# Performance work log

Hardware: AMD Instinct MI355X
Metric: run time of the kernel (lower is better)

The kernel has to match this reference:

```python
import jax, jax.numpy as jnp
import numpy as np

ALPHA = 0.7
EPS = 1e-12


def setup_inputs() -> dict:
    key = jax.random.key(0)
    k1, k2, k3, k4 = jax.random.split(key, 4)
    B, P, D = 4, 256, 384  # dinov2_vits14: 224/14=16 -> 256 patches, dim 384
    N, M = 100000, 2000    # local memory bank (max_memory), global bank (train images)
    return {
        "patches": jax.random.normal(k1, (B, P, D), dtype=jnp.float32),
        "globals_x": jax.random.normal(k2, (B, D), dtype=jnp.float32),
        "mb_local": jax.random.normal(k3, (N, D), dtype=jnp.float32),
        "mb_global": jax.random.normal(k4, (M, D), dtype=jnp.float32),
    }


def _l2_normalize(x):
    return x / (jnp.linalg.norm(x, axis=-1, keepdims=True) + EPS)


def reference(patches, globals_x, mb_local, mb_global):
    # Token normalization as in _extract_patch_tokens / _extract_global
    p = _l2_normalize(patches)    # [B, P, D]
    g = _l2_normalize(globals_x)  # [B, D]

    # Local: Euclidean cdist(p_i, MB_local) via gram trick, min over bank, max over patches
    p_sq = jnp.sum(p * p, axis=-1)                      # [B, P]
    mbl_sq = jnp.sum(mb_local * mb_local, axis=-1)      # [N]
    d2 = (p_sq[..., None] + mbl_sq[None, None, :]
          - 2.0 * jnp.einsum('bpd,nd->bpn', p, mb_local))  # [B, P, N]
    d = jnp.sqrt(jnp.maximum(d2, 0.0))
    local_score = jnp.max(jnp.min(d, axis=2), axis=1)   # [B]

    # Global: cdist(g_i, MB_global).min()
    g_sq = jnp.sum(g * g, axis=-1)                      # [B]
    mbg_sq = jnp.sum(mb_global * mb_global, axis=-1)    # [M]
    gd2 = g_sq[:, None] + mbg_sq[None, :] - 2.0 * (g @ mb_global.T)  # [B, M]
    gdist = jnp.min(jnp.sqrt(jnp.maximum(gd2, 0.0)), axis=1)         # [B]

    return ALPHA * local_score + (1.0 - ALPHA) * gdist  # [B] anomaly scores
```

## Files before the change

kernel.cpp:

```cpp
#include <hip/hip_runtime.h>
#include <math.h>


#define D 384
#define PQ 256
#define TNP 128
#define BK 64
#define LROW 72

typedef __attribute__((ext_vector_type(8))) short short8v;
typedef __attribute__((ext_vector_type(4))) float f32x4;

static __device__ __forceinline__ unsigned short f2bf(float f) {
  unsigned u = __float_as_uint(f);
  unsigned r = 0x7FFFu + ((u >> 16) & 1u);
  return (unsigned short)((u + r) >> 16);
}
static __device__ __forceinline__ unsigned pack2(float lo, float hi) {
  return (unsigned)f2bf(lo) | ((unsigned)f2bf(hi) << 16);
}

__global__ void prep_kernel(const float* __restrict__ patches,
                            const float* __restrict__ globals_x,
                            float* __restrict__ pf32,
                            unsigned short* __restrict__ pbf,
                            float* __restrict__ psq,
                            float* __restrict__ gf32,
                            float* __restrict__ gsq,
                            int Q) {
  const int row = blockIdx.x;
  const int lane = threadIdx.x;
  const float* src = (row < Q) ? (patches + (size_t)row * D)
                               : (globals_x + (size_t)(row - Q) * D);
  float v[6];
  float ss = 0.f;
#pragma unroll
  for (int j = 0; j < 6; ++j) { v[j] = src[lane + 64 * j]; ss += v[j] * v[j]; }
#pragma unroll
  for (int d = 1; d < 64; d <<= 1) ss += __shfl_xor(ss, d);
  const float inv = 1.f / (sqrtf(ss) + 1e-12f);
  float pn[6]; float ps = 0.f;
#pragma unroll
  for (int j = 0; j < 6; ++j) { pn[j] = v[j] * inv; ps += pn[j] * pn[j]; }
#pragma unroll
  for (int d = 1; d < 64; d <<= 1) ps += __shfl_xor(ps, d);
  if (row < Q) {
#pragma unroll
    for (int j = 0; j < 6; ++j) {
      pf32[(size_t)row * D + lane + 64 * j] = pn[j];
      pbf[(size_t)row * D + lane + 64 * j] = f2bf(pn[j]);
    }
    if (lane == 0) psq[row] = ps;
  } else {
    const int b = row - Q;
#pragma unroll
    for (int j = 0; j < 6; ++j) gf32[(size_t)b * D + lane + 64 * j] = pn[j];
    if (lane == 0) gsq[b] = ps;
  }
}

__device__ __forceinline__ void atomic_fmin(float* addr, float val) {
  unsigned* ua = (unsigned*)addr;
  float cur = __uint_as_float(atomicAdd(ua, 0u));
  while (val < cur) {
    unsigned assumed = __float_as_uint(cur);
    unsigned old = atomicCAS(ua, assumed, __float_as_uint(val));
    if (old == assumed) break;
    cur = __uint_as_float(old);
  }
}

template <int MODE>
__global__ __launch_bounds__(256, 2) void score_kernel(
    const float* __restrict__ mbl,
    const unsigned short* __restrict__ pbf,
    float* __restrict__ tilemin,
    int Q, int N, int QP, int q8, int r8) {
  __shared__ alignas(16) unsigned short lB0[TNP * LROW];
  __shared__ alignas(16) unsigned short lB1[TNP * LROW];
  __shared__ float msqH[TNP * 2];
  __shared__ float msqF[TNP];

  const int tid = threadIdx.x;
  const int lane = tid & 63;
  const int wid = tid >> 6;
  const int fr = lane & 15;
  const int g = lane >> 4;

  const int flat = blockIdx.x;
  const int xcd = flat & 7, idx = flat >> 3;
  const int wg = (xcd < r8 ? xcd * (q8 + 1) : r8 * (q8 + 1) + (xcd - r8) * q8) + idx;
  const int nb = wg / QP;
  const int qp = wg - nb * QP;
  const int qbase = qp * PQ;
  const int nbase = nb * TNP;

  const int brow = tid >> 1, h = tid & 1;
  const int gn = nbase + brow;
  const float* bptr = mbl + (size_t)((gn < N) ? gn : 0) * D + h * 32;
  const int boff = brow * LROW + h * 32;

  const unsigned short* abase = pbf + (size_t)(qbase + wid * 64 + fr) * D + g * 8;

  f32x4 acc[4][8];
#pragma unroll
  for (int i = 0; i < 4; ++i)
#pragma unroll
    for (int j = 0; j < 8; ++j) acc[i][j] = (f32x4){0.f, 0.f, 0.f, 0.f};
  float msqreg = 0.f;
  float4 breg[8];
  short8v a[8];

  auto bload = [&](int kc) {
    const float* src = bptr + kc * BK;
#pragma unroll
    for (int i = 0; i < 8; ++i) breg[i] = *(const float4*)(src + i * 4);
  };
  auto bwrite = [&](unsigned short* base) {
    float s = 0.f;
    uint4 w[4];
#pragma unroll
    for (int i = 0; i < 4; ++i) {
      float4 f0 = breg[2 * i], f1 = breg[2 * i + 1];
      s += f0.x*f0.x + f0.y*f0.y + f0.z*f0.z + f0.w*f0.w
         + f1.x*f1.x + f1.y*f1.y + f1.z*f1.z + f1.w*f1.w;
      w[i] = (uint4){ pack2(f0.x,f0.y), pack2(f0.z,f0.w), pack2(f1.x,f1.y), pack2(f1.z,f1.w) };
    }
#pragma unroll
    for (int i = 0; i < 4; ++i) *(uint4*)(base + boff + i * 8) = w[i];
    msqreg += s;
  };
  auto aload = [&](int kc) {
#pragma unroll
    for (int ks = 0; ks < 2; ++ks)
#pragma unroll
      for (int mf = 0; mf < 4; ++mf)
        a[ks * 4 + mf] = *(const short8v*)(abase + (size_t)mf * 16 * D + kc * BK + ks * 32);
  };
  auto compute = [&](const unsigned short* buf) {
#pragma unroll
    for (int ks = 0; ks < 2; ++ks) {
      short8v b[8];
#pragma unroll
      for (int nf = 0; nf < 8; ++nf)
        b[nf] = *(const short8v*)(&buf[(nf * 16 + fr) * LROW + (ks * 4 + g) * 8]);
#pragma unroll
      for (int mf = 0; mf < 4; ++mf)
#pragma unroll
        for (int nf = 0; nf < 8; ++nf)
          acc[mf][nf] = __builtin_amdgcn_mfma_f32_16x16x32_bf16(a[ks * 4 + mf], b[nf],
                                                                acc[mf][nf], 0, 0, 0);
    }
  };

  bload(0);
  bwrite(lB0);
  __syncthreads();
  aload(0); bload(1); compute(lB0); bwrite(lB1); __syncthreads();
  aload(1); bload(2); compute(lB1); bwrite(lB0); __syncthreads();
  aload(2); bload(3); compute(lB0); bwrite(lB1); __syncthreads();
  aload(3); bload(4); compute(lB1); bwrite(lB0); __syncthreads();
  aload(4); bload(5); compute(lB0); bwrite(lB1); __syncthreads();
  aload(5);           compute(lB1);              __syncthreads();

  msqH[tid] = msqreg;
  __syncthreads();
  if (tid < TNP) msqF[tid] = (nbase + tid < N) ? (msqH[2 * tid] + msqH[2 * tid + 1]) : 1e30f;
  __syncthreads();

  float mq[8];
#pragma unroll
  for (int nf = 0; nf < 8; ++nf) mq[nf] = msqF[nf * 16 + fr];

#pragma unroll
  for (int mf = 0; mf < 4; ++mf) {
#pragma unroll
    for (int j = 0; j < 4; ++j) {
      float v[4];
#pragma unroll
      for (int s = 0; s < 4; ++s)
        v[s] = fminf(mq[2 * s] - 2.f * acc[mf][2 * s][j],
                     mq[2 * s + 1] - 2.f * acc[mf][2 * s + 1][j]);
#pragma unroll
      for (int d2 = 1; d2 < 16; d2 <<= 1)
#pragma unroll
        for (int s = 0; s < 4; ++s) v[s] = fminf(v[s], __shfl_xor(v[s], d2));
      if (fr == 0) {
        const int q = qbase + wid * 64 + mf * 16 + g * 4 + j;
        if (MODE == 0) {
#pragma unroll
          for (int s = 0; s < 4; ++s)
            tilemin[(size_t)(nb * 4 + s) * Q + q] = v[s];
        } else {
          atomic_fmin(&tilemin[q],
                      fminf(fminf(v[0], v[1]), fminf(v[2], v[3])));
        }
      }
    }
  }
}

__global__ void init_inf_kernel(float* __restrict__ p, int n) {
  int i = blockIdx.x * 256 + threadIdx.x;
  if (i < n) p[i] = 1e30f;
}
__global__ void final_dmin_kernel(const float* __restrict__ d2min,
                                  const float* __restrict__ psq,
                                  float* __restrict__ dmin, int Q) {
  int q = blockIdx.x * 256 + threadIdx.x;
  if (q < Q) dmin[q] = sqrtf(fmaxf(psq[q] + d2min[q], 0.f));
}

__global__ __launch_bounds__(256) void transpose_kernel(
    const float* __restrict__ tm, float* __restrict__ tmT, int Q, int NSUBP) {
  __shared__ float t[64][65];
  const int tx = threadIdx.x & 63, ty = threadIdx.x >> 6;
  const int qb = blockIdx.x * 64, sb = blockIdx.y * 64;
#pragma unroll
  for (int i = 0; i < 64; i += 4)
    t[i + ty][tx] = tm[(size_t)(sb + i + ty) * Q + qb + tx];
  __syncthreads();
#pragma unroll
  for (int i = 0; i < 64; i += 4)
    tmT[(size_t)(qb + i + ty) * NSUBP + sb + tx] = t[tx][i + ty];
}

__device__ __forceinline__ float block_min(float v, float* red) {
#pragma unroll
  for (int d = 1; d < 64; d <<= 1) v = fminf(v, __shfl_xor(v, d));
  if ((threadIdx.x & 63) == 0) red[threadIdx.x >> 6] = v;
  __syncthreads();
  const float r = fminf(fminf(red[0], red[1]), fminf(red[2], red[3]));
  __syncthreads();
  return r;
}
__device__ __forceinline__ float block_max(float v, float* red) {
#pragma unroll
  for (int d = 1; d < 64; d <<= 1) v = fmaxf(v, __shfl_xor(v, d));
  if ((threadIdx.x & 63) == 0) red[threadIdx.x >> 6] = v;
  __syncthreads();
  const float r = fmaxf(fmaxf(red[0], red[1]), fmaxf(red[2], red[3]));
  __syncthreads();
  return r;
}

__global__ __launch_bounds__(256) void refine_kernel(
    const float* __restrict__ mbl,
    const float* __restrict__ pf32,
    const float* __restrict__ psq,
    const float* __restrict__ tmT,
    float* __restrict__ dmin,
    int Q, int N, int NSUB, int NSUBP) {
  __shared__ int cnt;
  __shared__ int cand[64];
  __shared__ float red[4];
  const int q = blockIdx.x;
  const int tid = threadIdx.x;
  if (tid == 0) cnt = 0;
  __syncthreads();

  const float* rowp = tmT + (size_t)q * NSUBP;
  float m = 1e30f;
  for (int r = tid; r < NSUB; r += 256) m = fminf(m, rowp[r]);
  const float gm = block_min(m, red);
  const float thr = gm + 0.25f;

  for (int r = tid; r < NSUB; r += 256)
    if (rowp[r] <= thr) { int i = atomicAdd(&cnt, 1); if (i < 64) cand[i] = r; }
  __syncthreads();
  const int nc = min(cnt, 64);

  const int row8 = tid >> 3, oct = tid & 7;
  const float* prow = pf32 + (size_t)q * D + oct * 48;
  float4 pr[12];
#pragma unroll
  for (int i = 0; i < 12; ++i) pr[i] = *(const float4*)(prow + i * 4);

  float best = 1e30f;
  for (int c = 0; c < nc; ++c) {
    const int n = cand[c] * 32 + row8;
    float v;
    if (n < N) {
      const float* mr = mbl + (size_t)n * D + oct * 48;
      float dot = 0.f, ms = 0.f;
#pragma unroll
      for (int i = 0; i < 12; ++i) {
        float4 aa = *(const float4*)(mr + i * 4);
        dot += aa.x*pr[i].x + aa.y*pr[i].y + aa.z*pr[i].z + aa.w*pr[i].w;
        ms  += aa.x*aa.x + aa.y*aa.y + aa.z*aa.z + aa.w*aa.w;
      }
      v = ms - 2.f * dot;
    } else {
      v = 1e30f;
    }
#pragma unroll
    for (int d2 = 1; d2 < 8; d2 <<= 1) {
      float o = __shfl_xor(v, d2);
      v = (n < N) ? v + o : 1e30f;
    }
    best = fminf(best, v);
  }
  best = block_min(best, red);
  if (tid == 0) dmin[q] = sqrtf(fmaxf(psq[q] + best, 0.f));
}

__global__ __launch_bounds__(256) void gmin_kernel(
    const float* __restrict__ mbg,
    const float* __restrict__ gf32,
    const float* __restrict__ gsq,
    float* __restrict__ gpartG,
    int M) {
  __shared__ float red[4];
  const int b = blockIdx.x, s = blockIdx.y;
  const int tid = threadIdx.x;
  const int sl = (M + 31) / 32;
  const int row = s * sl + tid;
  const float* g = gf32 + (size_t)b * D;
  float v = 1e30f;
  if (tid < sl && row < M) {
    const float* mr = mbg + (size_t)row * D;
    float dot = 0.f, ms = 0.f;
#pragma unroll 4
    for (int k = 0; k < D; k += 4) {
      float4 aa = *(const float4*)(mr + k);
      float4 p = *(const float4*)(g + k);
      dot += aa.x*p.x + aa.y*p.y + aa.z*p.z + aa.w*p.w;
      ms  += aa.x*aa.x + aa.y*aa.y + aa.z*aa.z + aa.w*aa.w;
    }
    v = gsq[b] + ms - 2.f * dot;
  }
  v = block_min(v, red);
  if (tid == 0) gpartG[b * 32 + s] = v;
}

__global__ __launch_bounds__(256) void out_kernel(
    const float* __restrict__ gpartG,
    const float* __restrict__ dmin,
    float* __restrict__ out,
    int P) {
  __shared__ float red[4];
  const int b = blockIdx.x;
  const int tid = threadIdx.x;
  float v = (tid < P) ? dmin[(size_t)b * P + tid] : -1e30f;
  const float local = block_max(v, red);
  float gm = (tid < 32) ? gpartG[b * 32 + tid] : 1e30f;
  gm = block_min(gm, red);
  if (tid == 0) out[b] = 0.7f * local + 0.3f * sqrtf(fmaxf(gm, 0.f));
}

extern "C" void kernel_launch(void* const* d_in, const int* in_sizes, int n_in,
                              void* d_out, int out_size, void* d_ws, size_t ws_size,
                              hipStream_t stream) {
  const float* patches   = (const float*)d_in[0];
  const float* globals_x = (const float*)d_in[1];
  const float* mbl       = (const float*)d_in[2];
  const float* mbg       = (const float*)d_in[3];
  float* out = (float*)d_out;

  const int Q = in_sizes[0] / D;
  const int B = in_sizes[1] / D;
  const int N = in_sizes[2] / D;
  const int M = in_sizes[3] / D;
  const int P = Q / B;
  const int NPAN = (N + TNP - 1) / TNP;
  const int NSUB = NPAN * 4;
  const int NSUBP = ((NSUB + 63) / 64) * 64;
  const int QP = (Q + PQ - 1) / PQ;
  const int nwg = QP * NPAN;
  const int q8 = nwg / 8, r8 = nwg % 8;

  char* w = (char*)d_ws;
  char* wend = (char*)d_ws + ws_size;
  auto alloc = [&](size_t bytes) {
    char* p = w;
    w += (bytes + 255) & ~(size_t)255;
    return p;
  };
  float*          pf32   = (float*)alloc((size_t)Q * D * sizeof(float));
  unsigned short* pbf    = (unsigned short*)alloc((size_t)Q * D * sizeof(unsigned short));
  float*          psq    = (float*)alloc((size_t)Q * sizeof(float));
  float*          gf32   = (float*)alloc((size_t)B * D * sizeof(float));
  float*          gsqp   = (float*)alloc((size_t)B * sizeof(float));
  float*          dmin   = (float*)alloc((size_t)Q * sizeof(float));
  float*          gpartG = (float*)alloc((size_t)B * 32 * sizeof(float));
  float*          d2min  = (float*)alloc((size_t)Q * sizeof(float));
  if (w > wend) return;

  const size_t tm_bytes = (size_t)NSUBP * Q * sizeof(float);
  const int full = (w + 2 * ((tm_bytes + 255) & ~(size_t)255) <= wend) ? 1 : 0;

  prep_kernel<<<Q + B, 64, 0, stream>>>(patches, globals_x, pf32, pbf, psq, gf32, gsqp, Q);

  if (full) {
    float* tilemin  = (float*)alloc(tm_bytes);
    float* tileminT = (float*)alloc(tm_bytes);
    score_kernel<0><<<nwg, 256, 0, stream>>>(mbl, pbf, tilemin, Q, N, QP, q8, r8);
    transpose_kernel<<<dim3(Q / 64, NSUBP / 64), 256, 0, stream>>>(tilemin, tileminT, Q, NSUBP);
    refine_kernel<<<Q, 256, 0, stream>>>(mbl, pf32, psq, tileminT, dmin, Q, N, NSUB, NSUBP);
  } else {
    init_inf_kernel<<<(Q + 255) / 256, 256, 0, stream>>>(d2min, Q);
    score_kernel<1><<<nwg, 256, 0, stream>>>(mbl, pbf, d2min, Q, N, QP, q8, r8);
    final_dmin_kernel<<<(Q + 255) / 256, 256, 0, stream>>>(d2min, psq, dmin, Q);
  }

  gmin_kernel<<<dim3(B, 32), 256, 0, stream>>>(mbg, gf32, gsqp, gpartG, M);
  out_kernel<<<B, 256, 0, stream>>>(gpartG, dmin, out, P);
}
```

Baseline: 491.7 us.

## Write tile minima in query-major layout and drop the transpose kernel

The score kernel now stores its four per-subtile minima as one float4 per query row, in query-major order, so the refine kernel can read them directly. This removes the separate transpose kernel, its extra buffer, and one full write and read of the tile-min matrix. The B-fragment loads in the MFMA loop are also split into two halves of four to cut live registers. The float4 stores are strided across queries and may coalesce less well than the old row-contiguous writes.

Result: faster. 457.4 us (-7.0%).

```diff
diff --git a/kernel.cpp b/kernel.cpp
--- a/kernel.cpp
+++ b/kernel.cpp
@@ -75,7 +75,7 @@
     const float* __restrict__ mbl,
     const unsigned short* __restrict__ pbf,
     float* __restrict__ tilemin,
-    int Q, int N, int QP, int q8, int r8) {
+    int Q, int N, int NSUBP, int QP, int q8, int r8) {
   __shared__ alignas(16) unsigned short lB0[TNP * LROW];
   __shared__ alignas(16) unsigned short lB1[TNP * LROW];
   __shared__ float msqH[TNP * 2];
@@ -140,16 +140,19 @@
   auto compute = [&](const unsigned short* buf) {
 #pragma unroll
     for (int ks = 0; ks < 2; ++ks) {
-      short8v b[8];
-#pragma unroll
-      for (int nf = 0; nf < 8; ++nf)
-        b[nf] = *(const short8v*)(&buf[(nf * 16 + fr) * LROW + (ks * 4 + g) * 8]);
-#pragma unroll
-      for (int mf = 0; mf < 4; ++mf)
-#pragma unroll
-        for (int nf = 0; nf < 8; ++nf)
-          acc[mf][nf] = __builtin_amdgcn_mfma_f32_16x16x32_bf16(a[ks * 4 + mf], b[nf],
-                                                                acc[mf][nf], 0, 0, 0);
+#pragma unroll
+      for (int half = 0; half < 2; ++half) {
+        short8v b4[4];
+#pragma unroll
+        for (int nf = 0; nf < 4; ++nf)
+          b4[nf] = *(const short8v*)(&buf[((half * 4 + nf) * 16 + fr) * LROW + (ks * 4 + g) * 8]);
+#pragma unroll
+        for (int mf = 0; mf < 4; ++mf)
+#pragma unroll
+          for (int nf = 0; nf < 4; ++nf)
+            acc[mf][half * 4 + nf] = __builtin_amdgcn_mfma_f32_16x16x32_bf16(
+                a[ks * 4 + mf], b4[nf], acc[mf][half * 4 + nf], 0, 0, 0);
+      }
     }
   };
 
@@ -188,9 +191,8 @@
       if (fr == 0) {
         const int q = qbase + wid * 64 + mf * 16 + g * 4 + j;
         if (MODE == 0) {
-#pragma unroll
-          for (int s = 0; s < 4; ++s)
-            tilemin[(size_t)(nb * 4 + s) * Q + q] = v[s];
+          *(float4*)&tilemin[(size_t)q * NSUBP + nb * 4] =
+              (float4){v[0], v[1], v[2], v[3]};
         } else {
           atomic_fmin(&tilemin[q],
                       fminf(fminf(v[0], v[1]), fminf(v[2], v[3])));
@@ -211,20 +213,6 @@
   if (q < Q) dmin[q] = sqrtf(fmaxf(psq[q] + d2min[q], 0.f));
 }
 
-__global__ __launch_bounds__(256) void transpose_kernel(
-    const float* __restrict__ tm, float* __restrict__ tmT, int Q, int NSUBP) {
-  __shared__ float t[64][65];
-  const int tx = threadIdx.x & 63, ty = threadIdx.x >> 6;
-  const int qb = blockIdx.x * 64, sb = blockIdx.y * 64;
-#pragma unroll
-  for (int i = 0; i < 64; i += 4)
-    t[i + ty][tx] = tm[(size_t)(sb + i + ty) * Q + qb + tx];
-  __syncthreads();
-#pragma unroll
-  for (int i = 0; i < 64; i += 4)
-    tmT[(size_t)(qb + i + ty) * NSUBP + sb + tx] = t[tx][i + ty];
-}
-
 __device__ __forceinline__ float block_min(float v, float* red) {
 #pragma unroll
   for (int d = 1; d < 64; d <<= 1) v = fminf(v, __shfl_xor(v, d));
@@ -248,7 +236,7 @@
     const float* __restrict__ mbl,
     const float* __restrict__ pf32,
     const float* __restrict__ psq,
-    const float* __restrict__ tmT,
+    const float* __restrict__ tm,
     float* __restrict__ dmin,
     int Q, int N, int NSUB, int NSUBP) {
   __shared__ int cnt;
@@ -259,7 +247,7 @@
   if (tid == 0) cnt = 0;
   __syncthreads();
 
-  const float* rowp = tmT + (size_t)q * NSUBP;
+  const float* rowp = tm + (size_t)q * NSUBP;
   float m = 1e30f;
   for (int r = tid; r < NSUB; r += 256) m = fminf(m, rowp[r]);
   const float gm = block_min(m, red);
@@ -386,20 +374,18 @@
   float*          d2min  = (float*)alloc((size_t)Q * sizeof(float));
   if (w > wend) return;
 
-  const size_t tm_bytes = (size_t)NSUBP * Q * sizeof(float);
-  const int full = (w + 2 * ((tm_bytes + 255) & ~(size_t)255) <= wend) ? 1 : 0;
+  const size_t tm_bytes = (size_t)Q * NSUBP * sizeof(float);
+  const int full = (w + ((tm_bytes + 255) & ~(size_t)255) <= wend) ? 1 : 0;
 
   prep_kernel<<<Q + B, 64, 0, stream>>>(patches, globals_x, pf32, pbf, psq, gf32, gsqp, Q);
 
   if (full) {
-    float* tilemin  = (float*)alloc(tm_bytes);
-    float* tileminT = (float*)alloc(tm_bytes);
-    score_kernel<0><<<nwg, 256, 0, stream>>>(mbl, pbf, tilemin, Q, N, QP, q8, r8);
-    transpose_kernel<<<dim3(Q / 64, NSUBP / 64), 256, 0, stream>>>(tilemin, tileminT, Q, NSUBP);
-    refine_kernel<<<Q, 256, 0, stream>>>(mbl, pf32, psq, tileminT, dmin, Q, N, NSUB, NSUBP);
+    float* tilemin = (float*)alloc(tm_bytes);
+    score_kernel<0><<<nwg, 256, 0, stream>>>(mbl, pbf, tilemin, Q, N, NSUBP, QP, q8, r8);
+    refine_kernel<<<Q, 256, 0, stream>>>(mbl, pf32, psq, tilemin, dmin, Q, N, NSUB, NSUBP);
   } else {
     init_inf_kernel<<<(Q + 255) / 256, 256, 0, stream>>>(d2min, Q);
-    score_kernel<1><<<nwg, 256, 0, stream>>>(mbl, pbf, d2min, Q, N, QP, q8, r8);
+    score_kernel<1><<<nwg, 256, 0, stream>>>(mbl, pbf, d2min, Q, N, NSUBP, QP, q8, r8);
     final_dmin_kernel<<<(Q + 255) / 256, 256, 0, stream>>>(d2min, psq, dmin, Q);
   }
 
```
